# Optimization experiments

Measured on AMD Instinct MI355X. Metric: run time of the kernel, lower is better.

The kernel has to match this reference:

```python
import jax, jax.numpy as jnp
import numpy as np

N = 163842   # icosahedron level-7 vertices
CH = 64
EPS = 1e-5
SLOPE = 0.2

def _bn_lrelu(x, g, b):
    # BatchNorm1d over vertex dim (training-mode batch stats, biased var) + LeakyReLU(0.2)
    mu = jnp.mean(x, axis=0)
    var = jnp.var(x, axis=0)
    y = (x - mu) * jax.lax.rsqrt(var + EPS) * g + b
    return jnp.where(y > 0, y, SLOPE * y)

def _onering_conv(x, neigh, W, bias):
    # gather 7 one-ring neighbors per vertex, flatten, linear project
    n = x.shape[0]
    feat = x[neigh].reshape(n, -1)          # [N, 7*C]
    return feat @ W + bias                  # [N, out]

def setup_inputs() -> dict:
    key = jax.random.key(0)
    ks = jax.random.split(key, 8)
    d = {
        "x": jax.random.normal(ks[0], (N, CH), jnp.float32),
        "neigh_orders": jax.random.randint(ks[1], (7 * N,), 0, N, jnp.int64),
    }
    for i, k in enumerate([1, 2, 3, 4]):
        cin = CH * k
        d[f"g{k}"] = jnp.ones((cin,), jnp.float32)
        d[f"b{k}"] = jnp.zeros((cin,), jnp.float32)
        d[f"W{k}"] = jax.random.normal(ks[2 + i], (7 * cin, CH), jnp.float32) * (1.0 / np.sqrt(7 * cin))
        d[f"wb{k}"] = jnp.zeros((CH,), jnp.float32)
    return d

def reference(x, neigh_orders, g1, b1, g2, b2, g3, b3, g4, b4,
              W1, wb1, W2, wb2, W3, wb3, W4, wb4):
    x1 = _onering_conv(_bn_lrelu(x, g1, b1), neigh_orders, W1, wb1)
    c2 = jnp.concatenate((x, x1), axis=1)
    x2 = _onering_conv(_bn_lrelu(c2, g2, b2), neigh_orders, W2, wb2)
    c3 = jnp.concatenate((x, x1, x2), axis=1)
    x3 = _onering_conv(_bn_lrelu(c3, g3, b3), neigh_orders, W3, wb3)
    c4 = jnp.concatenate((x, x1, x2, x3), axis=1)
    x4 = _onering_conv(_bn_lrelu(c4, g4, b4), neigh_orders, W4, wb4)
    return x4
```

## Files before the change

### kernel.cpp

```cpp
#include <hip/hip_runtime.h>
#include <stdint.h>

#define NV 163842
#define EPSV 1e-5f

using short8 = __attribute__((ext_vector_type(8))) short;
using f32x4  = __attribute__((ext_vector_type(4))) float;

static __device__ __forceinline__ unsigned short f2bf(float f) {
    union { float f; unsigned int i; } v; v.f = f;
    return (unsigned short)((v.i + 0x7FFFu + ((v.i >> 16) & 1u)) >> 16);
}
static __device__ __forceinline__ void bf2x(unsigned int w, float& a, float& b) {
    union { unsigned int i; float f; } lo, hi;
    lo.i = w << 16; hi.i = w & 0xFFFF0000u;
    a = lo.f; b = hi.f;
}
static __device__ __forceinline__ unsigned int pack2(float a, float b) {
    union { float f; unsigned int i; } ua, ub; ua.f = a; ub.f = b;
    return __builtin_amdgcn_perm(ub.i + 0x8000u, ua.i + 0x8000u, 0x07060302);
}

__global__ __launch_bounds__(256) void k_zero(float* __restrict__ ACC) {
    ACC[threadIdx.x] = 0.f;
    ACC[256 + threadIdx.x] = 0.f;
}

__global__ __launch_bounds__(256) void k_cast(const float* __restrict__ x,
                                              unsigned short* __restrict__ C,
                                              float* __restrict__ ACC) {
    const int t = threadIdx.x;
    const int wv = t >> 6, lane = t & 63;
    const int v = blockIdx.x * 64 + (t >> 2);
    const int c0 = (t & 3) * 16;
    float f[16];
    const bool valid = v < NV;
    if (valid) {
        const float4* p = (const float4*)(x + (size_t)v * 64 + c0);
#pragma unroll
        for (int i = 0; i < 4; ++i) {
            float4 q = p[i];
            f[i * 4 + 0] = q.x; f[i * 4 + 1] = q.y; f[i * 4 + 2] = q.z; f[i * 4 + 3] = q.w;
        }
        unsigned int o[8];
#pragma unroll
        for (int i = 0; i < 8; ++i)
            o[i] = ((unsigned int)f2bf(f[2 * i])) | (((unsigned int)f2bf(f[2 * i + 1])) << 16);
        uint4* dst = (uint4*)(C + (size_t)v * 256 + c0);
        dst[0] = uint4{o[0], o[1], o[2], o[3]};
        dst[1] = uint4{o[4], o[5], o[6], o[7]};
    } else {
#pragma unroll
        for (int i = 0; i < 16; ++i) f[i] = 0.f;
    }
    float s[16], s2[16];
#pragma unroll
    for (int i = 0; i < 16; ++i) { s[i] = f[i]; s2[i] = f[i] * f[i]; }
#pragma unroll
    for (int mask = 4; mask <= 32; mask <<= 1) {
#pragma unroll
        for (int i = 0; i < 16; ++i) {
            s[i]  += __shfl_xor(s[i],  mask);
            s2[i] += __shfl_xor(s2[i], mask);
        }
    }
    __shared__ float red[4 * 128];
    if ((lane >> 2) == 0) {
        int cb = (lane & 3) * 16;
#pragma unroll
        for (int i = 0; i < 16; ++i) {
            red[wv * 128 + cb + i]      = s[i];
            red[wv * 128 + 64 + cb + i] = s2[i];
        }
    }
    __syncthreads();
    if (t < 128) {
        float v4 = red[t] + red[128 + t] + red[256 + t] + red[384 + t];
        int c = t & 63, which = t >> 6;
        atomicAdd(&ACC[which * 256 + c], v4);
    }
}

__global__ __launch_bounds__(256) void k_wt_all(const float* __restrict__ W1,
                                                const float* __restrict__ W2,
                                                const float* __restrict__ W3,
                                                const float* __restrict__ W4,
                                                unsigned short* __restrict__ WT) {
    int j = blockIdx.x * 256 + threadIdx.x;
    if (j >= 286720) return;
    const float* W; int jj, K7;
    if (j < 28672)       { W = W1; jj = j;          K7 = 448;  }
    else if (j < 86016)  { W = W2; jj = j - 28672;  K7 = 896;  }
    else if (j < 172032) { W = W3; jj = j - 86016;  K7 = 1344; }
    else                 { W = W4; jj = j - 172032; K7 = 1792; }
    int n = jj / K7, k = jj - n * K7;
    WT[j] = f2bf(W[(size_t)k * 64 + n]);
}

template<int CIN, int GRP, bool FINAL>
__global__ __launch_bounds__(256) void k_gg(const unsigned short* __restrict__ C,
                                            const int* __restrict__ neigh,
                                            const unsigned short* __restrict__ WT,
                                            const float* __restrict__ g,
                                            const float* __restrict__ bglob,
                                            const float* __restrict__ wb,
                                            float* __restrict__ ACC,
                                            unsigned short* __restrict__ Cout,
                                            float* __restrict__ Fout) {
    constexpr int KB = CIN / 64;
    constexpr int NC = 7 * KB;
    constexpr int K7 = 7 * CIN;

    __shared__ float ssc[256], ssh[256];
    __shared__ int sIdx[896];
    __shared__ unsigned short sA[128 * 72];
    __shared__ unsigned short sW[64 * 72];

    const int t = threadIdx.x;
    const int v0 = blockIdx.x * 128;

    if (t < CIN) {
        float s = ACC[t], s2 = ACC[256 + t];
        float mu = s * (1.0f / NV);
        float var = fmaf(-mu, mu, s2 * (1.0f / NV));
        float sc = g[t] * rsqrtf(var + EPSV);
        ssc[t] = sc;
        ssh[t] = bglob[t] - mu * sc;
    }
    for (int q = t; q < 896; q += 256) {
        int gi = v0 * 7 + q;
        sIdx[q] = (gi < NV * 7) ? neigh[gi] : 0;
    }
    __syncthreads();

    const int wv = t >> 6, lane = t & 63;
    const int m = lane & 15, quad = lane >> 4;
    const int arow = t >> 1, ahalf = t & 1;
    const int wrow = t >> 2, wq = t & 3;

    f32x4 acc[2][4];
#pragma unroll
    for (int i = 0; i < 2; ++i)
#pragma unroll
        for (int j = 0; j < 4; ++j) acc[i][j] = f32x4{0.f, 0.f, 0.f, 0.f};

    auto load_chunk = [&](int c, uint4* aa, uint4& x0, uint4& x1) {
        int r = c / KB, kb = c - r * KB;
        int src = sIdx[arow * 7 + r];
        const uint4* pa = (const uint4*)(C + (size_t)src * 256 + kb * 64 + ahalf * 32);
        aa[0] = pa[0]; aa[1] = pa[1]; aa[2] = pa[2]; aa[3] = pa[3];
        const uint4* pw = (const uint4*)(WT + (size_t)wrow * K7 + c * 64 + wq * 16);
        x0 = pw[0]; x1 = pw[1];
    };
    auto stage = [&](const uint4* aa, uint4 x0, uint4 x1, int c) {
        int kb = c - (c / KB) * KB;
        int chb = kb * 64 + ahalf * 32;
        unsigned short* dstA = sA + arow * 72 + ahalf * 32;
#pragma unroll
        for (int i = 0; i < 4; ++i) {
            unsigned int u[4] = {aa[i].x, aa[i].y, aa[i].z, aa[i].w};
            unsigned int o[4];
#pragma unroll
            for (int jj = 0; jj < 4; ++jj) {
                float lo, hi; bf2x(u[jj], lo, hi);
                int ch = chb + i * 8 + jj * 2;
                float y0 = fmaf(lo, ssc[ch],     ssh[ch]);
                float y1 = fmaf(hi, ssc[ch + 1], ssh[ch + 1]);
                y0 = y0 > 0.f ? y0 : 0.2f * y0;
                y1 = y1 > 0.f ? y1 : 0.2f * y1;
                o[jj] = pack2(y0, y1);
            }
            *(uint4*)(dstA + i * 8) = uint4{o[0], o[1], o[2], o[3]};
        }
        *(uint4*)(sW + wrow * 72 + wq * 16)     = x0;
        *(uint4*)(sW + wrow * 72 + wq * 16 + 8) = x1;
    };

    uint4 a[4], w0, w1;
    load_chunk(0, a, w0, w1);
#pragma unroll 2
    for (int c = 0; c < NC; ++c) {
        uint4 na[4], nw0, nw1;
        if (c + 1 < NC) load_chunk(c + 1, na, nw0, nw1);
        stage(a, w0, w1, c);
        __syncthreads();
#pragma unroll
        for (int s = 0; s < 2; ++s) {
            short8 af0 = *(const short8*)(sA + (wv * 32 + m) * 72      + s * 32 + quad * 8);
            short8 af1 = *(const short8*)(sA + (wv * 32 + 16 + m) * 72 + s * 32 + quad * 8);
#pragma unroll
            for (int ct = 0; ct < 4; ++ct) {
                short8 bf = *(const short8*)(sW + (ct * 16 + m) * 72 + s * 32 + quad * 8);
                acc[0][ct] = __builtin_amdgcn_mfma_f32_16x16x32_bf16(af0, bf, acc[0][ct], 0, 0, 0);
                acc[1][ct] = __builtin_amdgcn_mfma_f32_16x16x32_bf16(af1, bf, acc[1][ct], 0, 0, 0);
            }
        }
        __syncthreads();
        if (c + 1 < NC) {
#pragma unroll
            for (int i = 0; i < 4; ++i) a[i] = na[i];
            w0 = nw0; w1 = nw1;
        }
    }

    float bsum[4]  = {0.f, 0.f, 0.f, 0.f};
    float b2sum[4] = {0.f, 0.f, 0.f, 0.f};
#pragma unroll
    for (int mt = 0; mt < 2; ++mt) {
#pragma unroll
        for (int ct = 0; ct < 4; ++ct) {
            int col = ct * 16 + m;
            float bv = wb[col];
#pragma unroll
            for (int j = 0; j < 4; ++j) {
                int vr = v0 + wv * 32 + mt * 16 + quad * 4 + j;
                float val = acc[mt][ct][j] + bv;
                if (vr < NV) {
                    if (FINAL) {
                        Fout[(size_t)vr * 64 + col] = val;
                    } else {
                        Cout[(size_t)vr * 256 + GRP * 64 + col] = f2bf(val);
                        bsum[ct] += val; b2sum[ct] += val * val;
                    }
                }
            }
        }
    }
    if (!FINAL) {
#pragma unroll
        for (int ct = 0; ct < 4; ++ct) {
            bsum[ct]  += __shfl_xor(bsum[ct], 16);
            bsum[ct]  += __shfl_xor(bsum[ct], 32);
            b2sum[ct] += __shfl_xor(b2sum[ct], 16);
            b2sum[ct] += __shfl_xor(b2sum[ct], 32);
        }
        float* red = (float*)sA;
        if (quad == 0) {
#pragma unroll
            for (int ct = 0; ct < 4; ++ct) {
                red[wv * 128 + ct * 16 + m]       = bsum[ct];
                red[512 + wv * 128 + ct * 16 + m] = b2sum[ct];
            }
        }
        __syncthreads();
        if (t < 128) {
            int c = t & 63, which = t >> 6;
            float v = red[which * 512 + c] + red[which * 512 + 128 + c] +
                      red[which * 512 + 256 + c] + red[which * 512 + 384 + c];
            atomicAdd(&ACC[which * 256 + GRP * 64 + c], v);
        }
    }
}

extern "C" void kernel_launch(void* const* d_in, const int* in_sizes, int n_in,
                              void* d_out, int out_size, void* d_ws, size_t ws_size,
                              hipStream_t stream) {
    const float* x     = (const float*)d_in[0];
    const int*   neigh = (const int*)d_in[1];
    const float* G[4]  = {(const float*)d_in[2],  (const float*)d_in[6],
                          (const float*)d_in[10], (const float*)d_in[14]};
    const float* B[4]  = {(const float*)d_in[3],  (const float*)d_in[7],
                          (const float*)d_in[11], (const float*)d_in[15]};
    const float* W[4]  = {(const float*)d_in[4],  (const float*)d_in[8],
                          (const float*)d_in[12], (const float*)d_in[16]};
    const float* WB[4] = {(const float*)d_in[5],  (const float*)d_in[9],
                          (const float*)d_in[13], (const float*)d_in[17]};
    float* out = (float*)d_out;

    char* ws = (char*)d_ws;
    size_t off = 0;
    unsigned short* C  = (unsigned short*)(ws + off); off += (size_t)NV * 256 * 2;
    unsigned short* WT = (unsigned short*)(ws + off); off += (size_t)286720 * 2;
    float* ACC         = (float*)(ws + off);          off += 512 * 4;

    k_zero<<<1, 256, 0, stream>>>(ACC);
    k_cast<<<(NV + 63) / 64, 256, 0, stream>>>(x, C, ACC);
    k_wt_all<<<(286720 + 255) / 256, 256, 0, stream>>>(W[0], W[1], W[2], W[3], WT);

    const int GG = (NV + 127) / 128;
    k_gg< 64, 1, false><<<GG, 256, 0, stream>>>(C, neigh, WT,          G[0], B[0], WB[0], ACC, C, nullptr);
    k_gg<128, 2, false><<<GG, 256, 0, stream>>>(C, neigh, WT + 28672,  G[1], B[1], WB[1], ACC, C, nullptr);
    k_gg<192, 3, false><<<GG, 256, 0, stream>>>(C, neigh, WT + 86016,  G[2], B[2], WB[2], ACC, C, nullptr);
    k_gg<256, 0, true ><<<GG, 256, 0, stream>>>(C, neigh, WT + 172032, G[3], B[3], WB[3], ACC, nullptr, out);
}
```

Before: 528.2 us.

## Pre-normalize activations and stage gathers via direct global-to-LDS loads

Moves BatchNorm+LeakyReLU out of the gather-GEMM into a separate per-layer normalization pass that writes a compact normalized bf16 buffer (CN). The GEMM kernel then loads the gathered neighbor rows and the weight tiles straight into LDS with global_load_lds, using an XOR-swizzled layout in place of register staging with padded rows. This removes the normalization that was repeated up to seven times per vertex and the register round-trip. In exchange it adds an extra full read/write pass per layer and drops the previous register prefetch of the next chunk, so loads and MFMA no longer overlap within a block.

```diff
diff --git a/kernel.cpp b/kernel.cpp
--- a/kernel.cpp
+++ b/kernel.cpp
@@ -19,6 +19,11 @@
 static __device__ __forceinline__ unsigned int pack2(float a, float b) {
     union { float f; unsigned int i; } ua, ub; ua.f = a; ub.f = b;
     return __builtin_amdgcn_perm(ub.i + 0x8000u, ua.i + 0x8000u, 0x07060302);
+}
+
+static __device__ __forceinline__ void gl_lds16(const unsigned short* g, unsigned short* l) {
+    __builtin_amdgcn_global_load_lds((__attribute__((address_space(1))) void*)g,
+                                     (__attribute__((address_space(3))) void*)l, 16, 0, 0);
 }
 
 __global__ __launch_bounds__(256) void k_zero(float* __restrict__ ACC) {
@@ -97,109 +102,111 @@
     WT[j] = f2bf(W[(size_t)k * 64 + n]);
 }
 
-template<int CIN, int GRP, bool FINAL>
-__global__ __launch_bounds__(256) void k_gg(const unsigned short* __restrict__ C,
-                                            const int* __restrict__ neigh,
-                                            const unsigned short* __restrict__ WT,
-                                            const float* __restrict__ g,
-                                            const float* __restrict__ bglob,
-                                            const float* __restrict__ wb,
-                                            float* __restrict__ ACC,
-                                            unsigned short* __restrict__ Cout,
-                                            float* __restrict__ Fout) {
-    constexpr int KB = CIN / 64;
-    constexpr int NC = 7 * KB;
-    constexpr int K7 = 7 * CIN;
-
+template<int CIN>
+__global__ __launch_bounds__(256) void k_norm(const unsigned short* __restrict__ C,
+                                              const float* __restrict__ ACC,
+                                              const float* __restrict__ g,
+                                              const float* __restrict__ b,
+                                              unsigned short* __restrict__ CN) {
     __shared__ float ssc[256], ssh[256];
-    __shared__ int sIdx[896];
-    __shared__ unsigned short sA[128 * 72];
-    __shared__ unsigned short sW[64 * 72];
-
     const int t = threadIdx.x;
-    const int v0 = blockIdx.x * 128;
-
     if (t < CIN) {
         float s = ACC[t], s2 = ACC[256 + t];
         float mu = s * (1.0f / NV);
         float var = fmaf(-mu, mu, s2 * (1.0f / NV));
         float sc = g[t] * rsqrtf(var + EPSV);
         ssc[t] = sc;
-        ssh[t] = bglob[t] - mu * sc;
-    }
+        ssh[t] = b[t] - mu * sc;
+    }
+    __syncthreads();
+    constexpr int C8 = CIN / 8;
+    const int total = NV * C8;
+    for (int idx = blockIdx.x * 256 + t; idx < total; idx += gridDim.x * 256) {
+        int v = idx / C8;
+        int c8 = idx - v * C8;
+        int ch = c8 * 8;
+        uint4 u = *(const uint4*)(C + (size_t)v * 256 + ch);
+        unsigned int in[4] = {u.x, u.y, u.z, u.w}, o[4];
+#pragma unroll
+        for (int j = 0; j < 4; ++j) {
+            float lo, hi; bf2x(in[j], lo, hi);
+            float y0 = fmaf(lo, ssc[ch + 2 * j],     ssh[ch + 2 * j]);
+            float y1 = fmaf(hi, ssc[ch + 2 * j + 1], ssh[ch + 2 * j + 1]);
+            y0 = y0 > 0.f ? y0 : 0.2f * y0;
+            y1 = y1 > 0.f ? y1 : 0.2f * y1;
+            o[j] = pack2(y0, y1);
+        }
+        *(uint4*)(CN + (size_t)v * CIN + ch) = uint4{o[0], o[1], o[2], o[3]};
+    }
+}
+
+template<int CIN, int GRP, bool FINAL>
+__global__ __launch_bounds__(256) void k_gg(const unsigned short* __restrict__ CN,
+                                            const int* __restrict__ neigh,
+                                            const unsigned short* __restrict__ WT,
+                                            const float* __restrict__ wb,
+                                            float* __restrict__ ACC,
+                                            unsigned short* __restrict__ Cout,
+                                            float* __restrict__ Fout) {
+    constexpr int KB = CIN / 64;
+    constexpr int K7 = 7 * CIN;
+
+    __shared__ int sIdx[896];
+    __shared__ unsigned short sA[128 * 64];
+    __shared__ unsigned short sW[64 * 64];
+
+    const int t = threadIdx.x;
+    const int v0 = blockIdx.x * 128;
+    const int wv = t >> 6, lane = t & 63;
+    const int m = lane & 15, quad = lane >> 4;
+    const int rowin = lane >> 3, slot = lane & 7;
+    const int sw = ((slot ^ rowin) * 8);
+
     for (int q = t; q < 896; q += 256) {
         int gi = v0 * 7 + q;
         sIdx[q] = (gi < NV * 7) ? neigh[gi] : 0;
     }
+
+    f32x4 acc[2][4];
+#pragma unroll
+    for (int i = 0; i < 2; ++i)
+#pragma unroll
+        for (int j = 0; j < 4; ++j) acc[i][j] = f32x4{0.f, 0.f, 0.f, 0.f};
+
     __syncthreads();
 
-    const int wv = t >> 6, lane = t & 63;
-    const int m = lane & 15, quad = lane >> 4;
-    const int arow = t >> 1, ahalf = t & 1;
-    const int wrow = t >> 2, wq = t & 3;
-
-    f32x4 acc[2][4];
-#pragma unroll
-    for (int i = 0; i < 2; ++i)
-#pragma unroll
-        for (int j = 0; j < 4; ++j) acc[i][j] = f32x4{0.f, 0.f, 0.f, 0.f};
-
-    auto load_chunk = [&](int c, uint4* aa, uint4& x0, uint4& x1) {
-        int r = c / KB, kb = c - r * KB;
-        int src = sIdx[arow * 7 + r];
-        const uint4* pa = (const uint4*)(C + (size_t)src * 256 + kb * 64 + ahalf * 32);
-        aa[0] = pa[0]; aa[1] = pa[1]; aa[2] = pa[2]; aa[3] = pa[3];
-        const uint4* pw = (const uint4*)(WT + (size_t)wrow * K7 + c * 64 + wq * 16);
-        x0 = pw[0]; x1 = pw[1];
-    };
-    auto stage = [&](const uint4* aa, uint4 x0, uint4 x1, int c) {
-        int kb = c - (c / KB) * KB;
-        int chb = kb * 64 + ahalf * 32;
-        unsigned short* dstA = sA + arow * 72 + ahalf * 32;
+    for (int r = 0; r < 7; ++r) {
+        const unsigned short* asrc[4];
 #pragma unroll
         for (int i = 0; i < 4; ++i) {
-            unsigned int u[4] = {aa[i].x, aa[i].y, aa[i].z, aa[i].w};
-            unsigned int o[4];
-#pragma unroll
-            for (int jj = 0; jj < 4; ++jj) {
-                float lo, hi; bf2x(u[jj], lo, hi);
-                int ch = chb + i * 8 + jj * 2;
-                float y0 = fmaf(lo, ssc[ch],     ssh[ch]);
-                float y1 = fmaf(hi, ssc[ch + 1], ssh[ch + 1]);
-                y0 = y0 > 0.f ? y0 : 0.2f * y0;
-                y1 = y1 > 0.f ? y1 : 0.2f * y1;
-                o[jj] = pack2(y0, y1);
-            }
-            *(uint4*)(dstA + i * 8) = uint4{o[0], o[1], o[2], o[3]};
-        }
-        *(uint4*)(sW + wrow * 72 + wq * 16)     = x0;
-        *(uint4*)(sW + wrow * 72 + wq * 16 + 8) = x1;
-    };
-
-    uint4 a[4], w0, w1;
-    load_chunk(0, a, w0, w1);
-#pragma unroll 2
-    for (int c = 0; c < NC; ++c) {
-        uint4 na[4], nw0, nw1;
-        if (c + 1 < NC) load_chunk(c + 1, na, nw0, nw1);
-        stage(a, w0, w1, c);
-        __syncthreads();
-#pragma unroll
-        for (int s = 0; s < 2; ++s) {
-            short8 af0 = *(const short8*)(sA + (wv * 32 + m) * 72      + s * 32 + quad * 8);
-            short8 af1 = *(const short8*)(sA + (wv * 32 + 16 + m) * 72 + s * 32 + quad * 8);
-#pragma unroll
-            for (int ct = 0; ct < 4; ++ct) {
-                short8 bf = *(const short8*)(sW + (ct * 16 + m) * 72 + s * 32 + quad * 8);
-                acc[0][ct] = __builtin_amdgcn_mfma_f32_16x16x32_bf16(af0, bf, acc[0][ct], 0, 0, 0);
-                acc[1][ct] = __builtin_amdgcn_mfma_f32_16x16x32_bf16(af1, bf, acc[1][ct], 0, 0, 0);
-            }
-        }
-        __syncthreads();
-        if (c + 1 < NC) {
-#pragma unroll
-            for (int i = 0; i < 4; ++i) a[i] = na[i];
-            w0 = nw0; w1 = nw1;
+            int gidx = sIdx[(wv * 32 + i * 8 + rowin) * 7 + r];
+            asrc[i] = CN + (size_t)gidx * CIN + sw;
+        }
+#pragma unroll
+        for (int kb = 0; kb < KB; ++kb) {
+            const int c = r * KB + kb;
+#pragma unroll
+            for (int i = 0; i < 4; ++i)
+                gl_lds16(asrc[i] + kb * 64, sA + (wv * 32 + i * 8) * 64);
+#pragma unroll
+            for (int j = 0; j < 2; ++j) {
+                int n = wv * 16 + j * 8 + rowin;
+                gl_lds16(WT + (size_t)n * K7 + c * 64 + sw, sW + (wv * 16 + j * 8) * 64);
+            }
+            __syncthreads();
+#pragma unroll
+            for (int s = 0; s < 2; ++s) {
+                const int sx = ((s * 4 + quad) ^ (m & 7)) * 8;
+                short8 af0 = *(const short8*)(sA + (wv * 32 + m) * 64      + sx);
+                short8 af1 = *(const short8*)(sA + (wv * 32 + 16 + m) * 64 + sx);
+#pragma unroll
+                for (int ct = 0; ct < 4; ++ct) {
+                    short8 bf = *(const short8*)(sW + (ct * 16 + m) * 64 + sx);
+                    acc[0][ct] = __builtin_amdgcn_mfma_f32_16x16x32_bf16(af0, bf, acc[0][ct], 0, 0, 0);
+                    acc[1][ct] = __builtin_amdgcn_mfma_f32_16x16x32_bf16(af1, bf, acc[1][ct], 0, 0, 0);
+                }
+            }
+            __syncthreads();
         }
     }
 
@@ -270,6 +277,7 @@
     char* ws = (char*)d_ws;
     size_t off = 0;
     unsigned short* C  = (unsigned short*)(ws + off); off += (size_t)NV * 256 * 2;
+    unsigned short* CN = (unsigned short*)(ws + off); off += (size_t)NV * 256 * 2;
     unsigned short* WT = (unsigned short*)(ws + off); off += (size_t)286720 * 2;
     float* ACC         = (float*)(ws + off);          off += 512 * 4;
 
@@ -278,8 +286,14 @@
     k_wt_all<<<(286720 + 255) / 256, 256, 0, stream>>>(W[0], W[1], W[2], W[3], WT);
 
     const int GG = (NV + 127) / 128;
-    k_gg< 64, 1, false><<<GG, 256, 0, stream>>>(C, neigh, WT,          G[0], B[0], WB[0], ACC, C, nullptr);
-    k_gg<128, 2, false><<<GG, 256, 0, stream>>>(C, neigh, WT + 28672,  G[1], B[1], WB[1], ACC, C, nullptr);
-    k_gg<192, 3, false><<<GG, 256, 0, stream>>>(C, neigh, WT + 86016,  G[2], B[2], WB[2], ACC, C, nullptr);
-    k_gg<256, 0, true ><<<GG, 256, 0, stream>>>(C, neigh, WT + 172032, G[3], B[3], WB[3], ACC, nullptr, out);
-}
+    const int NB = 2048;
+
+    k_norm< 64><<<NB, 256, 0, stream>>>(C, ACC, G[0], B[0], CN);
+    k_gg< 64, 1, false><<<GG, 256, 0, stream>>>(CN, neigh, WT,          WB[0], ACC, C, nullptr);
+    k_norm<128><<<NB, 256, 0, stream>>>(C, ACC, G[1], B[1], CN);
+    k_gg<128, 2, false><<<GG, 256, 0, stream>>>(CN, neigh, WT + 28672,  WB[1], ACC, C, nullptr);
+    k_norm<192><<<NB, 256, 0, stream>>>(C, ACC, G[2], B[2], CN);
+    k_gg<192, 3, false><<<GG, 256, 0, stream>>>(CN, neigh, WT + 86016,  WB[2], ACC, C, nullptr);
+    k_norm<256><<<NB, 256, 0, stream>>>(C, ACC, G[3], B[3], CN);
+    k_gg<256, 0, true ><<<GG, 256, 0, stream>>>(CN, neigh, WT + 172032, WB[3], ACC, nullptr, out);
+}
```

New measurement: 560.4 us. 1.06x slower.
